# Optimization experiments

Measured on AMD Instinct MI355X. Metric: run time of the kernel, lower is better.

## Reference

```python
import jax, jax.numpy as jnp
import numpy as np

N = 100000   # nodes
E = 1600000  # edges
EPS = 1e-5   # BatchNorm eps

def setup_inputs() -> dict:
    key = jax.random.key(0)
    ks = jax.random.split(key, 18)
    x = jax.random.normal(ks[0], (N, 128), jnp.float32)
    edge_index = jax.random.randint(ks[1], (2, E), 0, N, dtype=jnp.int64)
    # GCN layer weights (Glorot-ish scale) and biases
    W1 = jax.random.normal(ks[2], (128, 64), jnp.float32) * 0.1
    b1 = jnp.zeros((64,), jnp.float32)
    W2 = jax.random.normal(ks[3], (64, 64), jnp.float32) * 0.1
    b2 = jnp.zeros((64,), jnp.float32)
    W3 = jax.random.normal(ks[4], (64, 16), jnp.float32) * 0.1
    b3 = jnp.zeros((16,), jnp.float32)
    # BatchNorm (eval mode) affine params + running stats, 2 BN layers of width 64
    g1 = jax.random.uniform(ks[5], (64,), jnp.float32, 0.5, 1.5)
    be1 = jax.random.normal(ks[6], (64,), jnp.float32) * 0.1
    m1 = jax.random.normal(ks[7], (64,), jnp.float32) * 0.1
    v1 = jax.random.uniform(ks[8], (64,), jnp.float32, 0.5, 1.5)
    g2 = jax.random.uniform(ks[9], (64,), jnp.float32, 0.5, 1.5)
    be2 = jax.random.normal(ks[10], (64,), jnp.float32) * 0.1
    m2 = jax.random.normal(ks[11], (64,), jnp.float32) * 0.1
    v2 = jax.random.uniform(ks[12], (64,), jnp.float32, 0.5, 1.5)
    return {"x": x, "edge_index": edge_index,
            "W1": W1, "b1": b1, "W2": W2, "b2": b2, "W3": W3, "b3": b3,
            "g1": g1, "be1": be1, "m1": m1, "v1": v1,
            "g2": g2, "be2": be2, "m2": m2, "v2": v2}

def _gcn_graph(edge_index):
    # add self-loops, compute symmetric normalization deg^-1/2 * deg^-1/2
    loop = jnp.arange(N, dtype=edge_index.dtype)
    src = jnp.concatenate([edge_index[0], loop])
    dst = jnp.concatenate([edge_index[1], loop])
    deg = jax.ops.segment_sum(jnp.ones_like(dst, dtype=jnp.float32), dst, num_segments=N)
    dinv = jnp.where(deg > 0, jax.lax.rsqrt(jnp.maximum(deg, 1.0)), 0.0)
    norm = dinv[src] * dinv[dst]  # [E+N]
    return src, dst, norm

def reference(x, edge_index, W1, b1, W2, b2, W3, b3,
              g1, be1, m1, v1, g2, be2, m2, v2):
    src, dst, norm = _gcn_graph(edge_index)

    def conv(h, W, b):
        h = h @ W                              # [N, d_out]
        msg = h[src] * norm[:, None]           # gather + scale, [E+N, d_out]
        return jax.ops.segment_sum(msg, dst, num_segments=N) + b

    def bn(h, g, be, m, v):
        return g * (h - m) * jax.lax.rsqrt(v + EPS) + be

    h = jax.nn.relu(bn(conv(x, W1, b1), g1, be1, m1, v1))
    h = jax.nn.relu(bn(conv(h, W2, b2), g2, be2, m2, v2))
    return jax.nn.sigmoid(conv(h, W3, b3))
```

## Files before the change

kernel.cpp:

```cpp
#include <hip/hip_runtime.h>
#include <math.h>

#define NN 100000
#define NE 1600000
#define EPSBN 1e-5f
#define NBUCK 391

static __device__ __forceinline__ unsigned short f2bf(float f) {
    unsigned int u = __float_as_uint(f);
    u += 0x7fffu + ((u >> 16) & 1u);
    return (unsigned short)(u >> 16);
}
static __device__ __forceinline__ float bf2f(unsigned short s) {
    return __uint_as_float(((unsigned int)s) << 16);
}
static __device__ __forceinline__ void fma4(float4& a, float s, const float4& w) {
    a.x = fmaf(s, w.x, a.x); a.y = fmaf(s, w.y, a.y);
    a.z = fmaf(s, w.z, a.z); a.w = fmaf(s, w.w, a.w);
}
static __device__ __forceinline__ void fma2(float2& a, float s, const float2& w) {
    a.x = fmaf(s, w.x, a.x); a.y = fmaf(s, w.y, a.y);
}

__global__ __launch_bounds__(512) void init_small(int* __restrict__ bkcnt,
                                                  int* __restrict__ bcur) {
    int t = threadIdx.x;
    bkcnt[t] = 0;
    bcur[t] = 0;
}

__global__ __launch_bounds__(256) void bucket_count(const int* __restrict__ dst,
                                                    int* __restrict__ bkcnt) {
    __shared__ int lh[NBUCK];
    int t = threadIdx.x;
    for (int b = t; b < NBUCK; b += 256) lh[b] = 0;
    __syncthreads();
    int e0 = blockIdx.x * 4096;
#pragma unroll
    for (int i = 0; i < 16; ++i) {
        int e = e0 + i * 256 + t;
        if (e < NE) atomicAdd(&lh[dst[e] >> 8], 1);
    }
    __syncthreads();
    for (int b = t; b < NBUCK; b += 256)
        if (lh[b]) atomicAdd(&bkcnt[b], lh[b]);
}

__global__ __launch_bounds__(512) void scan2(const int* __restrict__ bkcnt,
                                             int* __restrict__ bb0) {
    __shared__ int sh[512];
    int t = threadIdx.x;
    int val = (t < NBUCK) ? bkcnt[t] : 0;
    sh[t] = val;
    __syncthreads();
    for (int off = 1; off < 512; off <<= 1) {
        int x = (t >= off) ? sh[t - off] : 0;
        __syncthreads();
        sh[t] += x;
        __syncthreads();
    }
    bb0[t] = sh[t] - val;
}

__global__ __launch_bounds__(256) void bin_kernel(const int* __restrict__ src,
                                                  const int* __restrict__ dst,
                                                  const int* __restrict__ bb0,
                                                  int* __restrict__ bcur,
                                                  unsigned int* __restrict__ bucketed) {
    __shared__ int lh[NBUCK];
    __shared__ int lbase[NBUCK];
    __shared__ int lcur[NBUCK];
    int t = threadIdx.x;
    for (int b = t; b < NBUCK; b += 256) lh[b] = 0;
    __syncthreads();
    int e0 = blockIdx.x * 4096;
#pragma unroll
    for (int i = 0; i < 16; ++i) {
        int e = e0 + i * 256 + t;
        if (e < NE) atomicAdd(&lh[dst[e] >> 8], 1);
    }
    __syncthreads();
    for (int b = t; b < NBUCK; b += 256) {
        lbase[b] = bb0[b] + atomicAdd(&bcur[b], lh[b]);
        lcur[b] = 0;
    }
    __syncthreads();
#pragma unroll
    for (int i = 0; i < 16; ++i) {
        int e = e0 + i * 256 + t;
        if (e < NE) {
            int d = dst[e], s = src[e];
            int b = d >> 8;
            int pos = lbase[b] + atomicAdd(&lcur[b], 1);
            bucketed[pos] = (unsigned int)s | ((unsigned int)(d & 255) << 24);
        }
    }
}

__global__ __launch_bounds__(256) void fine_scatter_fused(const unsigned int* __restrict__ bucketed,
                                                          const int* __restrict__ bb0,
                                                          int* __restrict__ row_start,
                                                          float* __restrict__ dinv,
                                                          int* __restrict__ sorted_src) {
    __shared__ int hist[256];
    __shared__ int sc[256];
    __shared__ int rsl[256];
    __shared__ int lcur[256];
    int b = blockIdx.x, t = threadIdx.x;
    hist[t] = 0; lcur[t] = 0;
    __syncthreads();
    int e0 = bb0[b], e1 = bb0[b + 1];
    for (int e = e0 + t; e < e1; e += 256)
        atomicAdd(&hist[bucketed[e] >> 24], 1);
    __syncthreads();
    int val = hist[t];
    sc[t] = val;
    __syncthreads();
    for (int off = 1; off < 256; off <<= 1) {
        int x = (t >= off) ? sc[t - off] : 0;
        __syncthreads();
        sc[t] += x;
        __syncthreads();
    }
    int ex = sc[t] - val;
    int node = b * 256 + t;
    if (node < NN) {
        row_start[node] = e0 + ex;
        dinv[node] = rsqrtf(1.0f + (float)val);
    }
    if (node == NN) row_start[NN] = NE;
    rsl[t] = e0 + ex;
    __syncthreads();
    for (int e = e0 + t; e < e1; e += 256) {
        unsigned int p = bucketed[e];
        int dl = (int)(p >> 24);
        int pos = rsl[dl] + atomicAdd(&lcur[dl], 1);
        sorted_src[pos] = (int)(p & 0xFFFFFFu);
    }
}

__global__ __launch_bounds__(256) void gemm_128_64_v3(const float* __restrict__ x,
                                                      const float* __restrict__ W,
                                                      const float* __restrict__ dinv,
                                                      unsigned short* __restrict__ hs) {
    __shared__ float xs[64][132];
    __shared__ float ws[128][64];
    int tid = threadIdx.x;
    int bn = blockIdx.x * 64;
    for (int id = tid; id < 2048; id += 256) {
        int r = id >> 4, c4 = id & 15;
        *(float4*)&ws[r][c4 * 4] = *(const float4*)(W + r * 64 + c4 * 4);
    }
    for (int id = tid; id < 64 * 33; id += 256) {
        int r = id / 33, c4 = id - r * 33;
        int n = bn + r; if (n >= NN) n = NN - 1;
        float4 v = make_float4(0.f, 0.f, 0.f, 0.f);
        if (c4 < 32) v = *(const float4*)(x + (size_t)n * 128 + c4 * 4);
        *(float4*)&xs[r][c4 * 4] = v;
    }
    __syncthreads();
    int tn = tid >> 4, tf = tid & 15;
    int f0 = tf * 4;
    float4 acc[4] = {{0,0,0,0},{0,0,0,0},{0,0,0,0},{0,0,0,0}};
#pragma unroll 2
    for (int k = 0; k < 128; k += 4) {
        float4 w0 = *(const float4*)&ws[k + 0][f0];
        float4 w1 = *(const float4*)&ws[k + 1][f0];
        float4 w2 = *(const float4*)&ws[k + 2][f0];
        float4 w3 = *(const float4*)&ws[k + 3][f0];
#pragma unroll
        for (int i = 0; i < 4; ++i) {
            float4 xa = *(const float4*)&xs[tn * 4 + i][k];
            fma4(acc[i], xa.x, w0); fma4(acc[i], xa.y, w1);
            fma4(acc[i], xa.z, w2); fma4(acc[i], xa.w, w3);
        }
    }
#pragma unroll
    for (int i = 0; i < 4; ++i) {
        int n = bn + tn * 4 + i;
        if (n < NN) {
            float di = dinv[n];
            ushort4 u;
            u.x = f2bf(acc[i].x * di); u.y = f2bf(acc[i].y * di);
            u.z = f2bf(acc[i].z * di); u.w = f2bf(acc[i].w * di);
            *(ushort4*)(hs + (size_t)n * 64 + f0) = u;
        }
    }
}

__global__ __launch_bounds__(256) void gemm_64_64_v3(const float* __restrict__ x,
                                                     const float* __restrict__ W,
                                                     const float* __restrict__ dinv,
                                                     unsigned short* __restrict__ hs) {
    __shared__ float xs[64][68];
    __shared__ float ws[64][64];
    int tid = threadIdx.x;
    int bn = blockIdx.x * 64;
    for (int id = tid; id < 1024; id += 256) {
        int r = id >> 4, c4 = id & 15;
        *(float4*)&ws[r][c4 * 4] = *(const float4*)(W + r * 64 + c4 * 4);
    }
    for (int id = tid; id < 64 * 17; id += 256) {
        int r = id / 17, c4 = id - r * 17;
        int n = bn + r; if (n >= NN) n = NN - 1;
        float4 v = make_float4(0.f, 0.f, 0.f, 0.f);
        if (c4 < 16) v = *(const float4*)(x + (size_t)n * 64 + c4 * 4);
        *(float4*)&xs[r][c4 * 4] = v;
    }
    __syncthreads();
    int tn = tid >> 4, tf = tid & 15;
    int f0 = tf * 4;
    float4 acc[4] = {{0,0,0,0},{0,0,0,0},{0,0,0,0},{0,0,0,0}};
#pragma unroll 2
    for (int k = 0; k < 64; k += 4) {
        float4 w0 = *(const float4*)&ws[k + 0][f0];
        float4 w1 = *(const float4*)&ws[k + 1][f0];
        float4 w2 = *(const float4*)&ws[k + 2][f0];
        float4 w3 = *(const float4*)&ws[k + 3][f0];
#pragma unroll
        for (int i = 0; i < 4; ++i) {
            float4 xa = *(const float4*)&xs[tn * 4 + i][k];
            fma4(acc[i], xa.x, w0); fma4(acc[i], xa.y, w1);
            fma4(acc[i], xa.z, w2); fma4(acc[i], xa.w, w3);
        }
    }
#pragma unroll
    for (int i = 0; i < 4; ++i) {
        int n = bn + tn * 4 + i;
        if (n < NN) {
            float di = dinv[n];
            ushort4 u;
            u.x = f2bf(acc[i].x * di); u.y = f2bf(acc[i].y * di);
            u.z = f2bf(acc[i].z * di); u.w = f2bf(acc[i].w * di);
            *(ushort4*)(hs + (size_t)n * 64 + f0) = u;
        }
    }
}

__global__ __launch_bounds__(256) void gemm_64_16_v3(const float* __restrict__ x,
                                                     const float* __restrict__ W,
                                                     const float* __restrict__ dinv,
                                                     unsigned short* __restrict__ hs) {
    __shared__ float xs[128][68];
    __shared__ float ws[64][16];
    int tid = threadIdx.x;
    int bn = blockIdx.x * 128;
    for (int id = tid; id < 256; id += 256) {
        int r = id >> 2, c4 = id & 3;
        *(float4*)&ws[r][c4 * 4] = *(const float4*)(W + r * 16 + c4 * 4);
    }
    for (int id = tid; id < 128 * 17; id += 256) {
        int r = id / 17, c4 = id - r * 17;
        int n = bn + r; if (n >= NN) n = NN - 1;
        float4 v = make_float4(0.f, 0.f, 0.f, 0.f);
        if (c4 < 16) v = *(const float4*)(x + (size_t)n * 64 + c4 * 4);
        *(float4*)&xs[r][c4 * 4] = v;
    }
    __syncthreads();
    int tn = tid >> 3, tf = tid & 7;
    int f0 = tf * 2;
    float2 acc[4] = {{0,0},{0,0},{0,0},{0,0}};
#pragma unroll 2
    for (int k = 0; k < 64; k += 4) {
        float2 w0 = *(const float2*)&ws[k + 0][f0];
        float2 w1 = *(const float2*)&ws[k + 1][f0];
        float2 w2 = *(const float2*)&ws[k + 2][f0];
        float2 w3 = *(const float2*)&ws[k + 3][f0];
#pragma unroll
        for (int i = 0; i < 4; ++i) {
            float4 xa = *(const float4*)&xs[tn * 4 + i][k];
            fma2(acc[i], xa.x, w0); fma2(acc[i], xa.y, w1);
            fma2(acc[i], xa.z, w2); fma2(acc[i], xa.w, w3);
        }
    }
#pragma unroll
    for (int i = 0; i < 4; ++i) {
        int n = bn + tn * 4 + i;
        if (n < NN) {
            float di = dinv[n];
            ushort2 u;
            u.x = f2bf(acc[i].x * di); u.y = f2bf(acc[i].y * di);
            *(ushort2*)(hs + (size_t)n * 16 + f0) = u;
        }
    }
}

__global__ __launch_bounds__(256) void csr_agg64_bn_relu(const int* __restrict__ rs,
                                                         const int* __restrict__ ss,
                                                         const unsigned short* __restrict__ hs,
                                                         const float* __restrict__ dinv,
                                                         const float* __restrict__ b,
                                                         const float* __restrict__ g,
                                                         const float* __restrict__ be,
                                                         const float* __restrict__ m,
                                                         const float* __restrict__ v,
                                                         float* __restrict__ out) {
    int lane = threadIdx.x & 63;
    int r = blockIdx.x * 4 + (threadIdx.x >> 6);
    int e0 = rs[r], e1 = rs[r + 1];
    float a0 = bf2f(hs[(size_t)r * 64 + lane]);
    float a1 = 0.f, a2 = 0.f, a3 = 0.f;
    for (int base = e0; base < e1; base += 64) {
        int nb = e1 - base; if (nb > 64) nb = 64;
        int sidx = (lane < nb) ? ss[base + lane] : 0;
        int j = 0;
        for (; j + 4 <= nb; j += 4) {
            int s0 = __shfl(sidx, j),     s1 = __shfl(sidx, j + 1);
            int s2 = __shfl(sidx, j + 2), s3 = __shfl(sidx, j + 3);
            a0 += bf2f(hs[(size_t)s0 * 64 + lane]);
            a1 += bf2f(hs[(size_t)s1 * 64 + lane]);
            a2 += bf2f(hs[(size_t)s2 * 64 + lane]);
            a3 += bf2f(hs[(size_t)s3 * 64 + lane]);
        }
        for (; j < nb; ++j)
            a0 += bf2f(hs[(size_t)__shfl(sidx, j) * 64 + lane]);
    }
    float acc = (a0 + a1) + (a2 + a3);
    float h = dinv[r] * acc + b[lane];
    h = g[lane] * (h - m[lane]) * rsqrtf(v[lane] + EPSBN) + be[lane];
    out[(size_t)r * 64 + lane] = fmaxf(h, 0.f);
}

__global__ __launch_bounds__(256) void csr_agg16_sigmoid(const int* __restrict__ rs,
                                                         const int* __restrict__ ss,
                                                         const unsigned short* __restrict__ hs,
                                                         const float* __restrict__ dinv,
                                                         const float* __restrict__ b,
                                                         float* __restrict__ out) {
    int lane = threadIdx.x & 63;
    int wid = blockIdx.x * 4 + (threadIdx.x >> 6);
    int grp = lane >> 4, fl = lane & 15;
    int r = wid * 4 + grp;
    int e0 = rs[r], e1 = rs[r + 1];
    float a0 = bf2f(hs[(size_t)r * 16 + fl]);
    float a1 = 0.f, a2 = 0.f, a3 = 0.f;
    for (int base = e0; base < e1; base += 16) {
        int nb = e1 - base; if (nb > 16) nb = 16;
        int sidx = (fl < nb) ? ss[base + fl] : 0;
        int j = 0;
        for (; j + 4 <= nb; j += 4) {
            int s0 = __shfl(sidx, grp * 16 + j),     s1 = __shfl(sidx, grp * 16 + j + 1);
            int s2 = __shfl(sidx, grp * 16 + j + 2), s3 = __shfl(sidx, grp * 16 + j + 3);
            a0 += bf2f(hs[(size_t)s0 * 16 + fl]);
            a1 += bf2f(hs[(size_t)s1 * 16 + fl]);
            a2 += bf2f(hs[(size_t)s2 * 16 + fl]);
            a3 += bf2f(hs[(size_t)s3 * 16 + fl]);
        }
        for (; j < nb; ++j)
            a0 += bf2f(hs[(size_t)__shfl(sidx, grp * 16 + j) * 16 + fl]);
    }
    float acc = (a0 + a1) + (a2 + a3);
    float h = dinv[r] * acc + b[fl];
    out[(size_t)r * 16 + fl] = 1.0f / (1.0f + expf(-h));
}

extern "C" void kernel_launch(void* const* d_in, const int* in_sizes, int n_in,
                              void* d_out, int out_size, void* d_ws, size_t ws_size,
                              hipStream_t stream) {
    const float* x   = (const float*)d_in[0];
    const int*   ei  = (const int*)d_in[1];
    const float* W1  = (const float*)d_in[2];
    const float* b1  = (const float*)d_in[3];
    const float* W2  = (const float*)d_in[4];
    const float* b2  = (const float*)d_in[5];
    const float* W3  = (const float*)d_in[6];
    const float* b3  = (const float*)d_in[7];
    const float* g1  = (const float*)d_in[8];
    const float* be1 = (const float*)d_in[9];
    const float* m1  = (const float*)d_in[10];
    const float* v1  = (const float*)d_in[11];
    const float* g2  = (const float*)d_in[12];
    const float* be2 = (const float*)d_in[13];
    const float* m2  = (const float*)d_in[14];
    const float* v2  = (const float*)d_in[15];
    float* out = (float*)d_out;

    const int* srcp = ei;
    const int* dstp = ei + NE;

    float* dinv = (float*)d_ws;
    float* A    = dinv + NN;
    unsigned short* Bh = (unsigned short*)(A + (size_t)NN * 64);
    int* row_start  = (int*)(Bh + (size_t)NN * 64);
    int* bkcnt      = row_start + NN + 2;
    int* bb0        = bkcnt + 512;
    int* bcur       = bb0 + 512;
    int* sorted_src = bcur + 512;
    unsigned int* bucketed = (unsigned int*)(sorted_src + NE);

    dim3 blk(256);
    int gBIN  = (NE + 4095) / 4096;
    int gG1   = (NN + 63) / 64;
    int gG3   = (NN + 127) / 128;
    int gA64  = NN / 4;
    int gA16  = NN / 16;

    init_small<<<1, 512, 0, stream>>>(bkcnt, bcur);
    bucket_count<<<gBIN, blk, 0, stream>>>(dstp, bkcnt);
    scan2<<<1, 512, 0, stream>>>(bkcnt, bb0);
    bin_kernel<<<gBIN, blk, 0, stream>>>(srcp, dstp, bb0, bcur, bucketed);
    fine_scatter_fused<<<NBUCK, blk, 0, stream>>>(bucketed, bb0, row_start, dinv, sorted_src);

    gemm_128_64_v3<<<gG1, blk, 0, stream>>>(x, W1, dinv, Bh);
    csr_agg64_bn_relu<<<gA64, blk, 0, stream>>>(row_start, sorted_src, Bh, dinv,
                                                b1, g1, be1, m1, v1, A);
    gemm_64_64_v3<<<gG1, blk, 0, stream>>>(A, W2, dinv, Bh);
    csr_agg64_bn_relu<<<gA64, blk, 0, stream>>>(row_start, sorted_src, Bh, dinv,
                                                b2, g2, be2, m2, v2, A);
    gemm_64_16_v3<<<gG3, blk, 0, stream>>>(A, W3, dinv, Bh);
    csr_agg16_sigmoid<<<gA16, blk, 0, stream>>>(row_start, sorted_src, Bh, dinv, b3, out);
}
```

Measured before the change: 361.1 us.

## Split each wavefront into edge sub-groups with vectorized bf16 gathers in CSR aggregation

The CSR aggregation kernels now split each 64-lane wavefront into sub-groups that process several edges at once. Each lane loads 4 (or 2) bf16 features with one vector load, and the partial sums are combined with xor-shuffle reductions. For the 16-wide layer, one row is now handled per wavefront with 8 groups of 8 lanes instead of 4 rows per wavefront. The aim is more memory-level parallelism and fewer, wider gather instructions. The cost is extra shuffle reductions and idle lanes in the epilogue and the tail, and the 16-wide layer launches more blocks.

```diff
diff --git a/kernel.cpp b/kernel.cpp
--- a/kernel.cpp
+++ b/kernel.cpp
@@ -13,6 +13,13 @@
 }
 static __device__ __forceinline__ float bf2f(unsigned short s) {
     return __uint_as_float(((unsigned int)s) << 16);
+}
+static __device__ __forceinline__ float4 bf4_to_f4(ushort4 u) {
+    float4 c; c.x = bf2f(u.x); c.y = bf2f(u.y); c.z = bf2f(u.z); c.w = bf2f(u.w);
+    return c;
+}
+static __device__ __forceinline__ void add4(float4& a, float4 c) {
+    a.x += c.x; a.y += c.y; a.z += c.z; a.w += c.w;
 }
 static __device__ __forceinline__ void fma4(float4& a, float s, const float4& w) {
     a.x = fmaf(s, w.x, a.x); a.y = fmaf(s, w.y, a.y);
@@ -285,73 +292,109 @@
     }
 }
 
-__global__ __launch_bounds__(256) void csr_agg64_bn_relu(const int* __restrict__ rs,
-                                                         const int* __restrict__ ss,
-                                                         const unsigned short* __restrict__ hs,
-                                                         const float* __restrict__ dinv,
-                                                         const float* __restrict__ b,
-                                                         const float* __restrict__ g,
-                                                         const float* __restrict__ be,
-                                                         const float* __restrict__ m,
-                                                         const float* __restrict__ v,
-                                                         float* __restrict__ out) {
+__global__ __launch_bounds__(256) void csr_agg64_v2(const int* __restrict__ rs,
+                                                    const int* __restrict__ ss,
+                                                    const unsigned short* __restrict__ hs,
+                                                    const float* __restrict__ dinv,
+                                                    const float* __restrict__ b,
+                                                    const float* __restrict__ g,
+                                                    const float* __restrict__ be,
+                                                    const float* __restrict__ m,
+                                                    const float* __restrict__ v,
+                                                    float* __restrict__ out) {
     int lane = threadIdx.x & 63;
     int r = blockIdx.x * 4 + (threadIdx.x >> 6);
+    int grp = lane >> 4, fl = lane & 15;
     int e0 = rs[r], e1 = rs[r + 1];
-    float a0 = bf2f(hs[(size_t)r * 64 + lane]);
-    float a1 = 0.f, a2 = 0.f, a3 = 0.f;
-    for (int base = e0; base < e1; base += 64) {
-        int nb = e1 - base; if (nb > 64) nb = 64;
-        int sidx = (lane < nb) ? ss[base + lane] : 0;
-        int j = 0;
-        for (; j + 4 <= nb; j += 4) {
-            int s0 = __shfl(sidx, j),     s1 = __shfl(sidx, j + 1);
-            int s2 = __shfl(sidx, j + 2), s3 = __shfl(sidx, j + 3);
-            a0 += bf2f(hs[(size_t)s0 * 64 + lane]);
-            a1 += bf2f(hs[(size_t)s1 * 64 + lane]);
-            a2 += bf2f(hs[(size_t)s2 * 64 + lane]);
-            a3 += bf2f(hs[(size_t)s3 * 64 + lane]);
-        }
-        for (; j < nb; ++j)
-            a0 += bf2f(hs[(size_t)__shfl(sidx, j) * 64 + lane]);
-    }
-    float acc = (a0 + a1) + (a2 + a3);
-    float h = dinv[r] * acc + b[lane];
-    h = g[lane] * (h - m[lane]) * rsqrtf(v[lane] + EPSBN) + be[lane];
-    out[(size_t)r * 64 + lane] = fmaxf(h, 0.f);
-}
-
-__global__ __launch_bounds__(256) void csr_agg16_sigmoid(const int* __restrict__ rs,
-                                                         const int* __restrict__ ss,
-                                                         const unsigned short* __restrict__ hs,
-                                                         const float* __restrict__ dinv,
-                                                         const float* __restrict__ b,
-                                                         float* __restrict__ out) {
+    float4 a0 = {0,0,0,0}, a1 = {0,0,0,0}, a2 = {0,0,0,0}, a3 = {0,0,0,0};
+    if (grp == 0)
+        a0 = bf4_to_f4(*(const ushort4*)(hs + (size_t)r * 64 + fl * 4));
+    int jj = e0;
+    for (; jj + 16 <= e1; jj += 16) {
+        int s0 = ss[jj + grp];
+        int s1 = ss[jj + 4 + grp];
+        int s2 = ss[jj + 8 + grp];
+        int s3 = ss[jj + 12 + grp];
+        ushort4 u0 = *(const ushort4*)(hs + (size_t)s0 * 64 + fl * 4);
+        ushort4 u1 = *(const ushort4*)(hs + (size_t)s1 * 64 + fl * 4);
+        ushort4 u2 = *(const ushort4*)(hs + (size_t)s2 * 64 + fl * 4);
+        ushort4 u3 = *(const ushort4*)(hs + (size_t)s3 * 64 + fl * 4);
+        add4(a0, bf4_to_f4(u0)); add4(a1, bf4_to_f4(u1));
+        add4(a2, bf4_to_f4(u2)); add4(a3, bf4_to_f4(u3));
+    }
+    for (; jj < e1; jj += 4) {
+        int idx = jj + grp;
+        if (idx < e1) {
+            int s = ss[idx];
+            add4(a1, bf4_to_f4(*(const ushort4*)(hs + (size_t)s * 64 + fl * 4)));
+        }
+    }
+    add4(a0, a1); add4(a2, a3); add4(a0, a2);
+    a0.x += __shfl_xor(a0.x, 16); a0.y += __shfl_xor(a0.y, 16);
+    a0.z += __shfl_xor(a0.z, 16); a0.w += __shfl_xor(a0.w, 16);
+    a0.x += __shfl_xor(a0.x, 32); a0.y += __shfl_xor(a0.y, 32);
+    a0.z += __shfl_xor(a0.z, 32); a0.w += __shfl_xor(a0.w, 32);
+    if (grp == 0) {
+        float di = dinv[r];
+        float4 bb = *(const float4*)(b + fl * 4);
+        float4 gg = *(const float4*)(g + fl * 4);
+        float4 bz = *(const float4*)(be + fl * 4);
+        float4 mm = *(const float4*)(m + fl * 4);
+        float4 vv = *(const float4*)(v + fl * 4);
+        float4 h;
+        h.x = fmaxf(gg.x * (di * a0.x + bb.x - mm.x) * rsqrtf(vv.x + EPSBN) + bz.x, 0.f);
+        h.y = fmaxf(gg.y * (di * a0.y + bb.y - mm.y) * rsqrtf(vv.y + EPSBN) + bz.y, 0.f);
+        h.z = fmaxf(gg.z * (di * a0.z + bb.z - mm.z) * rsqrtf(vv.z + EPSBN) + bz.z, 0.f);
+        h.w = fmaxf(gg.w * (di * a0.w + bb.w - mm.w) * rsqrtf(vv.w + EPSBN) + bz.w, 0.f);
+        *(float4*)(out + (size_t)r * 64 + fl * 4) = h;
+    }
+}
+
+__global__ __launch_bounds__(256) void csr_agg16_v2(const int* __restrict__ rs,
+                                                    const int* __restrict__ ss,
+                                                    const unsigned short* __restrict__ hs,
+                                                    const float* __restrict__ dinv,
+                                                    const float* __restrict__ b,
+                                                    float* __restrict__ out) {
     int lane = threadIdx.x & 63;
-    int wid = blockIdx.x * 4 + (threadIdx.x >> 6);
-    int grp = lane >> 4, fl = lane & 15;
-    int r = wid * 4 + grp;
+    int r = blockIdx.x * 4 + (threadIdx.x >> 6);
+    int grp = lane >> 3, fl = lane & 7;
     int e0 = rs[r], e1 = rs[r + 1];
-    float a0 = bf2f(hs[(size_t)r * 16 + fl]);
-    float a1 = 0.f, a2 = 0.f, a3 = 0.f;
-    for (int base = e0; base < e1; base += 16) {
-        int nb = e1 - base; if (nb > 16) nb = 16;
-        int sidx = (fl < nb) ? ss[base + fl] : 0;
-        int j = 0;
-        for (; j + 4 <= nb; j += 4) {
-            int s0 = __shfl(sidx, grp * 16 + j),     s1 = __shfl(sidx, grp * 16 + j + 1);
-            int s2 = __shfl(sidx, grp * 16 + j + 2), s3 = __shfl(sidx, grp * 16 + j + 3);
-            a0 += bf2f(hs[(size_t)s0 * 16 + fl]);
-            a1 += bf2f(hs[(size_t)s1 * 16 + fl]);
-            a2 += bf2f(hs[(size_t)s2 * 16 + fl]);
-            a3 += bf2f(hs[(size_t)s3 * 16 + fl]);
-        }
-        for (; j < nb; ++j)
-            a0 += bf2f(hs[(size_t)__shfl(sidx, grp * 16 + j) * 16 + fl]);
-    }
-    float acc = (a0 + a1) + (a2 + a3);
-    float h = dinv[r] * acc + b[fl];
-    out[(size_t)r * 16 + fl] = 1.0f / (1.0f + expf(-h));
+    float2 a0 = {0,0}, a1 = {0,0};
+    if (grp == 0) {
+        ushort2 u = *(const ushort2*)(hs + (size_t)r * 16 + fl * 2);
+        a0.x = bf2f(u.x); a0.y = bf2f(u.y);
+    }
+    int jj = e0;
+    for (; jj + 16 <= e1; jj += 16) {
+        int s0 = ss[jj + grp];
+        int s1 = ss[jj + 8 + grp];
+        ushort2 u0 = *(const ushort2*)(hs + (size_t)s0 * 16 + fl * 2);
+        ushort2 u1 = *(const ushort2*)(hs + (size_t)s1 * 16 + fl * 2);
+        a0.x += bf2f(u0.x); a0.y += bf2f(u0.y);
+        a1.x += bf2f(u1.x); a1.y += bf2f(u1.y);
+    }
+    for (; jj < e1; jj += 8) {
+        int idx = jj + grp;
+        if (idx < e1) {
+            int s = ss[idx];
+            ushort2 u = *(const ushort2*)(hs + (size_t)s * 16 + fl * 2);
+            a1.x += bf2f(u.x); a1.y += bf2f(u.y);
+        }
+    }
+    a0.x += a1.x; a0.y += a1.y;
+    a0.x += __shfl_xor(a0.x, 8);  a0.y += __shfl_xor(a0.y, 8);
+    a0.x += __shfl_xor(a0.x, 16); a0.y += __shfl_xor(a0.y, 16);
+    a0.x += __shfl_xor(a0.x, 32); a0.y += __shfl_xor(a0.y, 32);
+    if (grp == 0) {
+        float di = dinv[r];
+        float hx = di * a0.x + b[fl * 2];
+        float hy = di * a0.y + b[fl * 2 + 1];
+        float2 o;
+        o.x = 1.0f / (1.0f + expf(-hx));
+        o.y = 1.0f / (1.0f + expf(-hy));
+        *(float2*)(out + (size_t)r * 16 + fl * 2) = o;
+    }
 }
 
 extern "C" void kernel_launch(void* const* d_in, const int* in_sizes, int n_in,
@@ -392,8 +435,7 @@
     int gBIN  = (NE + 4095) / 4096;
     int gG1   = (NN + 63) / 64;
     int gG3   = (NN + 127) / 128;
-    int gA64  = NN / 4;
-    int gA16  = NN / 16;
+    int gA    = NN / 4;
 
     init_small<<<1, 512, 0, stream>>>(bkcnt, bcur);
     bucket_count<<<gBIN, blk, 0, stream>>>(dstp, bkcnt);
@@ -402,11 +444,11 @@
     fine_scatter_fused<<<NBUCK, blk, 0, stream>>>(bucketed, bb0, row_start, dinv, sorted_src);
 
     gemm_128_64_v3<<<gG1, blk, 0, stream>>>(x, W1, dinv, Bh);
-    csr_agg64_bn_relu<<<gA64, blk, 0, stream>>>(row_start, sorted_src, Bh, dinv,
-                                                b1, g1, be1, m1, v1, A);
+    csr_agg64_v2<<<gA, blk, 0, stream>>>(row_start, sorted_src, Bh, dinv,
+                                         b1, g1, be1, m1, v1, A);
     gemm_64_64_v3<<<gG1, blk, 0, stream>>>(A, W2, dinv, Bh);
-    csr_agg64_bn_relu<<<gA64, blk, 0, stream>>>(row_start, sorted_src, Bh, dinv,
-                                                b2, g2, be2, m2, v2, A);
+    csr_agg64_v2<<<gA, blk, 0, stream>>>(row_start, sorted_src, Bh, dinv,
+                                         b2, g2, be2, m2, v2, A);
     gemm_64_16_v3<<<gG3, blk, 0, stream>>>(A, W3, dinv, Bh);
-    csr_agg16_sigmoid<<<gA16, blk, 0, stream>>>(row_start, sorted_src, Bh, dinv, b3, out);
-}
+    csr_agg16_v2<<<gA, blk, 0, stream>>>(row_start, sorted_src, Bh, dinv, b3, out);
+}
```

Result: slower. 379.3 us (+5.0%).
